# Performance work log

Measured on AMD Instinct MI355X. Metric: run time of the kernel, lower is better.

The kernel has to match this reference:

```python
import jax, jax.numpy as jnp
import numpy as np

N = 10000      # nodes
E = 160000     # edges
D_IN = 512
D_H = 512
P_DROP = 0.2


def _glorot(key, shape):
    lim = float(np.sqrt(6.0 / (shape[0] + shape[1])))
    return jax.random.uniform(key, shape, jnp.float32, -lim, lim)


def setup_inputs() -> dict:
    key = jax.random.key(0)
    ks = jax.random.split(key, 8)
    h = jax.random.normal(ks[0], (N, D_IN), jnp.float32)
    src = jax.random.randint(ks[1], (E,), 0, N)
    dst = jax.random.randint(ks[2], (E,), 0, N)
    edge_weight = jax.random.uniform(ks[3], (E,), jnp.float32)
    W0 = _glorot(ks[4], (D_IN, D_H))
    W1 = _glorot(ks[5], (D_H, D_H))
    W2 = _glorot(ks[6], (D_H, D_H))
    b0 = jnp.zeros((D_H,), jnp.float32)
    b1 = jnp.zeros((D_H,), jnp.float32)
    b2 = jnp.zeros((D_H,), jnp.float32)
    return dict(h=h, src=src, dst=dst, edge_weight=edge_weight,
                W0=W0, b0=b0, W1=W1, b1=b1, W2=W2, b2=b2)


def _dropout(x, key):
    keep = jax.random.bernoulli(key, 1.0 - P_DROP, x.shape)
    return jnp.where(keep, x / (1.0 - P_DROP), 0.0)


def _graph_conv(x, src, dst, ew, W, b, act):
    # DGL GraphConv, norm='both', weight=True, bias=True, with edge_weight.
    ones = jnp.ones((src.shape[0],), x.dtype)
    deg_out = jnp.maximum(jax.ops.segment_sum(ones, src, num_segments=N), 1.0)
    deg_in = jnp.maximum(jax.ops.segment_sum(ones, dst, num_segments=N), 1.0)
    x = x * (deg_out ** -0.5)[:, None]          # src norm
    msg = x[src] * ew[:, None]                  # [E, D] gather + edge weight
    agg = jax.ops.segment_sum(msg, dst, num_segments=N)  # scatter-add
    out = (agg @ W) * (deg_in ** -0.5)[:, None] + b
    return act(out) if act is not None else out


def reference(h, src, dst, edge_weight, W0, b0, W1, b1, W2, b2):
    dk = jax.random.split(jax.random.key(42), 3)
    x = _dropout(h, dk[0])
    x = _graph_conv(x, src, dst, edge_weight, W0, b0, jax.nn.elu)
    x = _dropout(x, dk[1])
    x = _graph_conv(x, src, dst, edge_weight, W1, b1, jax.nn.elu)
    x = _dropout(x, dk[2])
    x = _graph_conv(x, src, dst, edge_weight, W2, b2, None)
    return x
```

## Files before the change

kernel.cpp:

```cpp
#include <hip/hip_runtime.h>
#include <stdint.h>

#define N_NODES 10000
#define N_EDGES 160000
#define D 512
#define TOT (N_NODES * D)
#define M_PAD 10112

typedef _Float16 h8 __attribute__((ext_vector_type(8)));
typedef float f4 __attribute__((ext_vector_type(4)));

__host__ __device__ inline uint32_t rotl32(uint32_t v, int r) {
    return (v << r) | (v >> (32 - r));
}

__host__ __device__ inline void tf2x32(uint32_t k0, uint32_t k1,
                                       uint32_t& x0, uint32_t& x1) {
    uint32_t k2 = k0 ^ k1 ^ 0x1BD11BDAu;
    x0 += k0; x1 += k1;
    x0 += x1; x1 = rotl32(x1, 13); x1 ^= x0;
    x0 += x1; x1 = rotl32(x1, 15); x1 ^= x0;
    x0 += x1; x1 = rotl32(x1, 26); x1 ^= x0;
    x0 += x1; x1 = rotl32(x1,  6); x1 ^= x0;
    x0 += k1; x1 += k2 + 1u;
    x0 += x1; x1 = rotl32(x1, 17); x1 ^= x0;
    x0 += x1; x1 = rotl32(x1, 29); x1 ^= x0;
    x0 += x1; x1 = rotl32(x1, 16); x1 ^= x0;
    x0 += x1; x1 = rotl32(x1, 24); x1 ^= x0;
    x0 += k2; x1 += k0 + 2u;
    x0 += x1; x1 = rotl32(x1, 13); x1 ^= x0;
    x0 += x1; x1 = rotl32(x1, 15); x1 ^= x0;
    x0 += x1; x1 = rotl32(x1, 26); x1 ^= x0;
    x0 += x1; x1 = rotl32(x1,  6); x1 ^= x0;
    x0 += k0; x1 += k1 + 3u;
    x0 += x1; x1 = rotl32(x1, 17); x1 ^= x0;
    x0 += x1; x1 = rotl32(x1, 29); x1 ^= x0;
    x0 += x1; x1 = rotl32(x1, 16); x1 ^= x0;
    x0 += x1; x1 = rotl32(x1, 24); x1 ^= x0;
    x0 += k1; x1 += k2 + 4u;
    x0 += x1; x1 = rotl32(x1, 13); x1 ^= x0;
    x0 += x1; x1 = rotl32(x1, 15); x1 ^= x0;
    x0 += x1; x1 = rotl32(x1, 26); x1 ^= x0;
    x0 += x1; x1 = rotl32(x1,  6); x1 ^= x0;
    x0 += k2; x1 += k0 + 5u;
}

__device__ __forceinline__ float dropout_gate(uint32_t k0, uint32_t k1, uint32_t j) {
    uint32_t c0 = 0u, c1 = j;
    tf2x32(k0, k1, c0, c1);
    uint32_t bits = c0 ^ c1;
    float u = __uint_as_float((bits >> 9) | 0x3f800000u) - 1.0f;
    return (u < 0.8f) ? 1.0f : 0.0f;
}

__device__ __forceinline__ void gl_lds16(const void* g, void* l) {
    __builtin_amdgcn_global_load_lds(
        (const __attribute__((address_space(1))) void*)g,
        (__attribute__((address_space(3))) void*)l, 16, 0, 0);
}

__global__ void hist_kernel(const int* __restrict__ src, const int* __restrict__ dst,
                            int* __restrict__ deg_out, int* __restrict__ deg_in) {
    int e = blockIdx.x * 256 + threadIdx.x;
    if (e >= N_EDGES) return;
    atomicAdd(&deg_out[src[e]], 1);
    atomicAdd(&deg_in[dst[e]], 1);
}

__global__ __launch_bounds__(1024)
void scan_kernel(const int* __restrict__ deg_in, const int* __restrict__ deg_out,
                 int* __restrict__ row_ptr,
                 float* __restrict__ rn_in, float* __restrict__ rn_out) {
    __shared__ int wsum[16];
    __shared__ int base_s;
    int tid = threadIdx.x;
    int lane = tid & 63, wv = tid >> 6;
    if (tid == 0) base_s = 0;
    __syncthreads();
    for (int start = 0; start < N_NODES; start += 1024) {
        int i = start + tid;
        int v = (i < N_NODES) ? deg_in[i] : 0;
        int s = v;
#pragma unroll
        for (int off = 1; off < 64; off <<= 1) {
            int t = __shfl_up(s, off, 64);
            if (lane >= off) s += t;
        }
        if (lane == 63) wsum[wv] = s;
        __syncthreads();
        if (wv == 0 && lane < 16) {
            int ws = wsum[lane];
#pragma unroll
            for (int off = 1; off < 16; off <<= 1) {
                int t = __shfl_up(ws, off, 64);
                if (lane >= off) ws += t;
            }
            wsum[lane] = ws;
        }
        __syncthreads();
        if (i < N_NODES) {
            int prefix = base_s + ((wv > 0) ? wsum[wv - 1] : 0) + (s - v);
            row_ptr[i] = prefix;
            rn_in[i]  = 1.0f / sqrtf(fmaxf((float)v, 1.0f));
            rn_out[i] = 1.0f / sqrtf(fmaxf((float)deg_out[i], 1.0f));
        }
        __syncthreads();
        if (tid == 0) base_s += wsum[15];
        __syncthreads();
    }
    if (tid == 0) row_ptr[N_NODES] = base_s;
}

__global__ void fill_kernel(const int* __restrict__ src, const int* __restrict__ dst,
                            const float* __restrict__ ew, const int* __restrict__ row_ptr,
                            int* __restrict__ cursor,
                            int* __restrict__ csr_src, float* __restrict__ csr_w) {
    int e = blockIdx.x * 256 + threadIdx.x;
    if (e >= N_EDGES) return;
    int v = dst[e];
    int pos = atomicAdd(&cursor[v], 1);
    int idx = row_ptr[v] + pos;
    csr_src[idx] = src[e];
    csr_w[idx] = ew[e];
}

__global__ __launch_bounds__(256)
void wconvert_kernel(const float* __restrict__ W0, const float* __restrict__ W1,
                     const float* __restrict__ W2, _Float16* __restrict__ Wt) {
    __shared__ float tile[64][65];
    const float* W = (blockIdx.z == 0) ? W0 : (blockIdx.z == 1) ? W1 : W2;
    _Float16* T = Wt + (size_t)blockIdx.z * 512 * 512;
    int r0 = blockIdx.y * 64, c0 = blockIdx.x * 64;
    int t = threadIdx.x;
    int c = t & 63, rq = t >> 6;
#pragma unroll
    for (int i = 0; i < 16; ++i) {
        int r = rq + i * 4;
        tile[r][c] = W[(size_t)(r0 + r) * 512 + c0 + c];
    }
    __syncthreads();
    int k = t & 63, nq = t >> 6;
#pragma unroll
    for (int i = 0; i < 16; ++i) {
        int n = nq + i * 4;
        T[(size_t)(c0 + n) * 512 + r0 + k] = (_Float16)tile[k][n];
    }
}

__global__ __launch_bounds__(256)
void dropout_kernel(const float* __restrict__ x, _Float16* __restrict__ y,
                    const float* __restrict__ rn_out, uint32_t k0, uint32_t k1) {
    int t = blockIdx.x * 256 + threadIdx.x;
    int j = t * 4;
    if (j >= TOT) return;
    float4 xv = *(const float4*)&x[j];
    float w = rn_out[j >> 9];
    _Float16 r[4];
    uint32_t jj = (uint32_t)j;
#pragma unroll
    for (int i = 0; i < 4; ++i) {
        float g = dropout_gate(k0, k1, jj + (uint32_t)i);
        float xi = (&xv.x)[i];
        r[i] = (_Float16)(g * (xi / 0.8f) * w);
    }
    *(ushort4*)&y[j] = *(ushort4*)r;
}

__global__ __launch_bounds__(256)
void aggregate_kernel(const _Float16* __restrict__ y, const int* __restrict__ row_ptr,
                      const int* __restrict__ csr_src, const float* __restrict__ csr_w,
                      _Float16* __restrict__ agg) {
    int node = blockIdx.x * 4 + (threadIdx.x >> 6);
    int lane = threadIdx.x & 63;
    if (node >= N_NODES) return;
    int beg = row_ptr[node], end = row_ptr[node + 1];
    float acc[8] = {0, 0, 0, 0, 0, 0, 0, 0};
    int k = beg;
    for (; k + 1 < end; k += 2) {
        int s0 = csr_src[k], s1 = csr_src[k + 1];
        float w0 = csr_w[k], w1 = csr_w[k + 1];
        h8 a = *(const h8*)&y[(size_t)s0 * 512 + lane * 8];
        h8 b = *(const h8*)&y[(size_t)s1 * 512 + lane * 8];
#pragma unroll
        for (int i = 0; i < 8; ++i) acc[i] += w0 * (float)a[i] + w1 * (float)b[i];
    }
    if (k < end) {
        int s0 = csr_src[k];
        float w0 = csr_w[k];
        h8 a = *(const h8*)&y[(size_t)s0 * 512 + lane * 8];
#pragma unroll
        for (int i = 0; i < 8; ++i) acc[i] += w0 * (float)a[i];
    }
    _Float16 r[8];
#pragma unroll
    for (int i = 0; i < 8; ++i) r[i] = (_Float16)acc[i];
    *(h8*)&agg[(size_t)node * 512 + lane * 8] = *(h8*)r;
}

__global__ __launch_bounds__(256)
void gemm_kernel(const _Float16* __restrict__ A, const _Float16* __restrict__ Wt,
                 const float* __restrict__ bias, const float* __restrict__ rn_in,
                 const float* __restrict__ rn_out,
                 _Float16* __restrict__ yout, float* __restrict__ fout,
                 int mode, uint32_t k0, uint32_t k1) {
    __shared__ _Float16 As[128 * 32];
    __shared__ _Float16 Bs[64 * 32];
    int tid = threadIdx.x;
    int wv = tid >> 6, lane = tid & 63;
    int row0 = blockIdx.y * 128, col0 = blockIdx.x * 64;
    int wr = wv >> 1, wc = wv & 1;

    f4 acc[4][2];
#pragma unroll
    for (int i = 0; i < 4; ++i)
#pragma unroll
        for (int j = 0; j < 2; ++j) acc[i][j] = (f4){0.f, 0.f, 0.f, 0.f};

    int kc = (lane & 3) * 8;
    const _Float16* pa0 = A + (size_t)(row0 + 32 * wv + (lane >> 2)) * 512 + kc;
    const _Float16* pa1 = pa0 + 16 * 512;
    const _Float16* pb  = Wt + (size_t)(col0 + 16 * wv + (lane >> 2)) * 512 + kc;
    _Float16* la0 = &As[(32 * wv) * 32];
    _Float16* la1 = &As[(32 * wv + 16) * 32];
    _Float16* lb  = &Bs[(16 * wv) * 32];

    int kf = (lane >> 4) * 8;
    const _Float16* fa = &As[(wr * 64 + (lane & 15)) * 32 + kf];
    const _Float16* fb = &Bs[(wc * 32 + (lane & 15)) * 32 + kf];

    for (int kk = 0; kk < 512; kk += 32) {
        gl_lds16(pa0 + kk, la0);
        gl_lds16(pa1 + kk, la1);
        gl_lds16(pb + kk, lb);
        __syncthreads();
        h8 af[4], bf[2];
#pragma unroll
        for (int mt = 0; mt < 4; ++mt) af[mt] = *(const h8*)(fa + mt * 16 * 32);
#pragma unroll
        for (int nt = 0; nt < 2; ++nt) bf[nt] = *(const h8*)(fb + nt * 16 * 32);
#pragma unroll
        for (int mt = 0; mt < 4; ++mt)
#pragma unroll
            for (int nt = 0; nt < 2; ++nt)
                acc[mt][nt] = __builtin_amdgcn_mfma_f32_16x16x32_f16(
                    af[mt], bf[nt], acc[mt][nt], 0, 0, 0);
        __syncthreads();
    }

    int mbase = row0 + wr * 64;
    int nbase = col0 + wc * 32;
#pragma unroll
    for (int mt = 0; mt < 4; ++mt) {
#pragma unroll
        for (int nt = 0; nt < 2; ++nt) {
            int gr0 = mbase + mt * 16 + (lane >> 4) * 4;
            int gc = nbase + nt * 16 + (lane & 15);
            float bcol = bias[gc];
#pragma unroll
            for (int i = 0; i < 4; ++i) {
                int gr = gr0 + i;
                if (gr >= N_NODES) continue;
                float v = acc[mt][nt][i] * rn_in[gr] + bcol;
                if (mode == 0) {
                    v = (v > 0.f) ? v : expm1f(v);
                    float g = dropout_gate(k0, k1, (uint32_t)(gr * 512 + gc));
                    v = g * (v / 0.8f) * rn_out[gr];
                    yout[(size_t)gr * 512 + gc] = (_Float16)v;
                } else {
                    fout[(size_t)gr * 512 + gc] = v;
                }
            }
        }
    }
}

extern "C" void kernel_launch(void* const* d_in, const int* in_sizes, int n_in,
                              void* d_out, int out_size, void* d_ws, size_t ws_size,
                              hipStream_t stream) {
    const float* h   = (const float*)d_in[0];
    const int*   src = (const int*)d_in[1];
    const int*   dst = (const int*)d_in[2];
    const float* ew  = (const float*)d_in[3];
    const float* W0  = (const float*)d_in[4];
    const float* b0  = (const float*)d_in[5];
    const float* W1  = (const float*)d_in[6];
    const float* b1  = (const float*)d_in[7];
    const float* W2  = (const float*)d_in[8];
    const float* b2  = (const float*)d_in[9];
    const float* bl[3] = {b0, b1, b2};
    float* out = (float*)d_out;

    char* ws = (char*)d_ws;
    _Float16* y16  = (_Float16*)ws; ws += (size_t)TOT * 2;
    _Float16* aggF = (_Float16*)ws; ws += (size_t)M_PAD * 512 * 2;
    _Float16* Wt   = (_Float16*)ws; ws += (size_t)3 * 512 * 512 * 2;
    int* degi_in  = (int*)ws;  ws += N_NODES * 4;
    int* degi_out = (int*)ws;  ws += N_NODES * 4;
    int* row_ptr  = (int*)ws;  ws += (N_NODES + 1) * 4;
    int* cursor   = (int*)ws;  ws += N_NODES * 4;
    int* csr_src  = (int*)ws;  ws += N_EDGES * 4;
    float* csr_w  = (float*)ws; ws += N_EDGES * 4;
    float* rn_in  = (float*)ws; ws += N_NODES * 4;
    float* rn_out = (float*)ws; ws += N_NODES * 4;

    hipMemsetAsync(degi_in, 0, N_NODES * 4, stream);
    hipMemsetAsync(degi_out, 0, N_NODES * 4, stream);
    hipMemsetAsync(cursor, 0, N_NODES * 4, stream);

    hist_kernel<<<(N_EDGES + 255) / 256, 256, 0, stream>>>(src, dst, degi_out, degi_in);
    scan_kernel<<<1, 1024, 0, stream>>>(degi_in, degi_out, row_ptr, rn_in, rn_out);
    fill_kernel<<<(N_EDGES + 255) / 256, 256, 0, stream>>>(src, dst, ew, row_ptr, cursor,
                                                           csr_src, csr_w);
    wconvert_kernel<<<dim3(8, 8, 3), 256, 0, stream>>>(W0, W1, W2, Wt);

    uint32_t dk[3][2];
    for (int i = 0; i < 3; ++i) {
        uint32_t c0 = 0u, c1 = (uint32_t)i;
        tf2x32(0u, 42u, c0, c1);
        dk[i][0] = c0; dk[i][1] = c1;
    }

    dropout_kernel<<<(TOT / 4 + 255) / 256, 256, 0, stream>>>(h, y16, rn_out,
                                                              dk[0][0], dk[0][1]);
    for (int l = 0; l < 3; ++l) {
        aggregate_kernel<<<N_NODES / 4, 256, 0, stream>>>(y16, row_ptr, csr_src,
                                                          csr_w, aggF);
        int mode = (l < 2) ? 0 : 1;
        uint32_t dk0 = (l < 2) ? dk[l + 1][0] : 0u;
        uint32_t dk1 = (l < 2) ? dk[l + 1][1] : 0u;
        gemm_kernel<<<dim3(512 / 64, M_PAD / 128), 256, 0, stream>>>(
            aggF, Wt + (size_t)l * 512 * 512, bl[l], rn_in, rn_out,
            y16, out, mode, dk0, dk1);
    }
}
```

Measured before the change: 327.3 us.

## Pack CSR edges as int2, unroll aggregation by four, widen GEMM K tile

CSR source index and edge weight are interleaved into one int2 array, so the aggregation reads one 8-byte load per edge. The gather loop is unrolled to four edges so more row loads are in flight at once. The GEMM K-tile grows from 32 to 64, halving the number of barrier-separated iterations at the cost of more LDS. The three memsets are merged into one by placing the counters next to each other.

```diff
diff --git a/kernel.cpp b/kernel.cpp
--- a/kernel.cpp
+++ b/kernel.cpp
@@ -113,15 +113,13 @@
 
 __global__ void fill_kernel(const int* __restrict__ src, const int* __restrict__ dst,
                             const float* __restrict__ ew, const int* __restrict__ row_ptr,
-                            int* __restrict__ cursor,
-                            int* __restrict__ csr_src, float* __restrict__ csr_w) {
+                            int* __restrict__ cursor, int2* __restrict__ csr) {
     int e = blockIdx.x * 256 + threadIdx.x;
     if (e >= N_EDGES) return;
     int v = dst[e];
     int pos = atomicAdd(&cursor[v], 1);
     int idx = row_ptr[v] + pos;
-    csr_src[idx] = src[e];
-    csr_w[idx] = ew[e];
+    csr[idx] = make_int2(src[e], __float_as_int(ew[e]));
 }
 
 __global__ __launch_bounds__(256)
@@ -168,26 +166,30 @@
 
 __global__ __launch_bounds__(256)
 void aggregate_kernel(const _Float16* __restrict__ y, const int* __restrict__ row_ptr,
-                      const int* __restrict__ csr_src, const float* __restrict__ csr_w,
-                      _Float16* __restrict__ agg) {
+                      const int2* __restrict__ csr, _Float16* __restrict__ agg) {
     int node = blockIdx.x * 4 + (threadIdx.x >> 6);
     int lane = threadIdx.x & 63;
     if (node >= N_NODES) return;
     int beg = row_ptr[node], end = row_ptr[node + 1];
     float acc[8] = {0, 0, 0, 0, 0, 0, 0, 0};
     int k = beg;
-    for (; k + 1 < end; k += 2) {
-        int s0 = csr_src[k], s1 = csr_src[k + 1];
-        float w0 = csr_w[k], w1 = csr_w[k + 1];
-        h8 a = *(const h8*)&y[(size_t)s0 * 512 + lane * 8];
-        h8 b = *(const h8*)&y[(size_t)s1 * 512 + lane * 8];
-#pragma unroll
-        for (int i = 0; i < 8; ++i) acc[i] += w0 * (float)a[i] + w1 * (float)b[i];
-    }
-    if (k < end) {
-        int s0 = csr_src[k];
-        float w0 = csr_w[k];
-        h8 a = *(const h8*)&y[(size_t)s0 * 512 + lane * 8];
+    for (; k + 3 < end; k += 4) {
+        int2 e0 = csr[k], e1 = csr[k + 1], e2 = csr[k + 2], e3 = csr[k + 3];
+        h8 a0 = *(const h8*)&y[(size_t)e0.x * 512 + lane * 8];
+        h8 a1 = *(const h8*)&y[(size_t)e1.x * 512 + lane * 8];
+        h8 a2 = *(const h8*)&y[(size_t)e2.x * 512 + lane * 8];
+        h8 a3 = *(const h8*)&y[(size_t)e3.x * 512 + lane * 8];
+        float w0 = __int_as_float(e0.y), w1 = __int_as_float(e1.y);
+        float w2 = __int_as_float(e2.y), w3 = __int_as_float(e3.y);
+#pragma unroll
+        for (int i = 0; i < 8; ++i)
+            acc[i] += w0 * (float)a0[i] + w1 * (float)a1[i]
+                    + w2 * (float)a2[i] + w3 * (float)a3[i];
+    }
+    for (; k < end; ++k) {
+        int2 e0 = csr[k];
+        float w0 = __int_as_float(e0.y);
+        h8 a = *(const h8*)&y[(size_t)e0.x * 512 + lane * 8];
 #pragma unroll
         for (int i = 0; i < 8; ++i) acc[i] += w0 * (float)a[i];
     }
@@ -197,14 +199,15 @@
     *(h8*)&agg[(size_t)node * 512 + lane * 8] = *(h8*)r;
 }
 
+#define GBK 64
 __global__ __launch_bounds__(256)
 void gemm_kernel(const _Float16* __restrict__ A, const _Float16* __restrict__ Wt,
                  const float* __restrict__ bias, const float* __restrict__ rn_in,
                  const float* __restrict__ rn_out,
                  _Float16* __restrict__ yout, float* __restrict__ fout,
                  int mode, uint32_t k0, uint32_t k1) {
-    __shared__ _Float16 As[128 * 32];
-    __shared__ _Float16 Bs[64 * 32];
+    __shared__ _Float16 As[128 * GBK];
+    __shared__ _Float16 Bs[64 * GBK];
     int tid = threadIdx.x;
     int wv = tid >> 6, lane = tid & 63;
     int row0 = blockIdx.y * 128, col0 = blockIdx.x * 64;
@@ -216,34 +219,41 @@
 #pragma unroll
         for (int j = 0; j < 2; ++j) acc[i][j] = (f4){0.f, 0.f, 0.f, 0.f};
 
-    int kc = (lane & 3) * 8;
-    const _Float16* pa0 = A + (size_t)(row0 + 32 * wv + (lane >> 2)) * 512 + kc;
-    const _Float16* pa1 = pa0 + 16 * 512;
-    const _Float16* pb  = Wt + (size_t)(col0 + 16 * wv + (lane >> 2)) * 512 + kc;
-    _Float16* la0 = &As[(32 * wv) * 32];
-    _Float16* la1 = &As[(32 * wv + 16) * 32];
-    _Float16* lb  = &Bs[(16 * wv) * 32];
+    int srow = lane >> 3;
+    int skc = (lane & 7) * 8;
+    const _Float16* pa = A + (size_t)(row0 + 32 * wv + srow) * 512 + skc;
+    const _Float16* pb = Wt + (size_t)(col0 + 16 * wv + srow) * 512 + skc;
+    _Float16* la = &As[(32 * wv) * GBK];
+    _Float16* lb = &Bs[(16 * wv) * GBK];
 
     int kf = (lane >> 4) * 8;
-    const _Float16* fa = &As[(wr * 64 + (lane & 15)) * 32 + kf];
-    const _Float16* fb = &Bs[(wc * 32 + (lane & 15)) * 32 + kf];
-
-    for (int kk = 0; kk < 512; kk += 32) {
-        gl_lds16(pa0 + kk, la0);
-        gl_lds16(pa1 + kk, la1);
-        gl_lds16(pb + kk, lb);
-        __syncthreads();
-        h8 af[4], bf[2];
-#pragma unroll
-        for (int mt = 0; mt < 4; ++mt) af[mt] = *(const h8*)(fa + mt * 16 * 32);
-#pragma unroll
-        for (int nt = 0; nt < 2; ++nt) bf[nt] = *(const h8*)(fb + nt * 16 * 32);
-#pragma unroll
-        for (int mt = 0; mt < 4; ++mt)
+    const _Float16* fa = &As[(wr * 64 + (lane & 15)) * GBK + kf];
+    const _Float16* fb = &Bs[(wc * 32 + (lane & 15)) * GBK + kf];
+
+    for (int kk = 0; kk < 512; kk += GBK) {
+#pragma unroll
+        for (int r = 0; r < 4; ++r)
+            gl_lds16(pa + (size_t)r * 8 * 512 + kk, la + (8 * r) * GBK);
+#pragma unroll
+        for (int r = 0; r < 2; ++r)
+            gl_lds16(pb + (size_t)r * 8 * 512 + kk, lb + (8 * r) * GBK);
+        __syncthreads();
+#pragma unroll
+        for (int ks = 0; ks < 2; ++ks) {
+            h8 af[4], bf[2];
+#pragma unroll
+            for (int mt = 0; mt < 4; ++mt)
+                af[mt] = *(const h8*)(fa + mt * 16 * GBK + ks * 32);
 #pragma unroll
             for (int nt = 0; nt < 2; ++nt)
-                acc[mt][nt] = __builtin_amdgcn_mfma_f32_16x16x32_f16(
-                    af[mt], bf[nt], acc[mt][nt], 0, 0, 0);
+                bf[nt] = *(const h8*)(fb + nt * 16 * GBK + ks * 32);
+#pragma unroll
+            for (int mt = 0; mt < 4; ++mt)
+#pragma unroll
+                for (int nt = 0; nt < 2; ++nt)
+                    acc[mt][nt] = __builtin_amdgcn_mfma_f32_16x16x32_f16(
+                        af[mt], bf[nt], acc[mt][nt], 0, 0, 0);
+        }
         __syncthreads();
     }
 
@@ -296,21 +306,19 @@
     _Float16* Wt   = (_Float16*)ws; ws += (size_t)3 * 512 * 512 * 2;
     int* degi_in  = (int*)ws;  ws += N_NODES * 4;
     int* degi_out = (int*)ws;  ws += N_NODES * 4;
+    int* cursor   = (int*)ws;  ws += N_NODES * 4;
     int* row_ptr  = (int*)ws;  ws += (N_NODES + 1) * 4;
-    int* cursor   = (int*)ws;  ws += N_NODES * 4;
-    int* csr_src  = (int*)ws;  ws += N_EDGES * 4;
-    float* csr_w  = (float*)ws; ws += N_EDGES * 4;
+    ws = (char*)(((uintptr_t)ws + 15) & ~(uintptr_t)15);
+    int2* csr     = (int2*)ws; ws += (size_t)N_EDGES * 8;
     float* rn_in  = (float*)ws; ws += N_NODES * 4;
     float* rn_out = (float*)ws; ws += N_NODES * 4;
 
-    hipMemsetAsync(degi_in, 0, N_NODES * 4, stream);
-    hipMemsetAsync(degi_out, 0, N_NODES * 4, stream);
-    hipMemsetAsync(cursor, 0, N_NODES * 4, stream);
+    hipMemsetAsync(degi_in, 0, 3 * N_NODES * 4, stream);
 
     hist_kernel<<<(N_EDGES + 255) / 256, 256, 0, stream>>>(src, dst, degi_out, degi_in);
     scan_kernel<<<1, 1024, 0, stream>>>(degi_in, degi_out, row_ptr, rn_in, rn_out);
-    fill_kernel<<<(N_EDGES + 255) / 256, 256, 0, stream>>>(src, dst, ew, row_ptr, cursor,
-                                                           csr_src, csr_w);
+    fill_kernel<<<(N_EDGES + 255) / 256, 256, 0, stream>>>(src, dst, ew, row_ptr,
+                                                           cursor, csr);
     wconvert_kernel<<<dim3(8, 8, 3), 256, 0, stream>>>(W0, W1, W2, Wt);
 
     uint32_t dk[3][2];
@@ -323,8 +331,7 @@
     dropout_kernel<<<(TOT / 4 + 255) / 256, 256, 0, stream>>>(h, y16, rn_out,
                                                               dk[0][0], dk[0][1]);
     for (int l = 0; l < 3; ++l) {
-        aggregate_kernel<<<N_NODES / 4, 256, 0, stream>>>(y16, row_ptr, csr_src,
-                                                          csr_w, aggF);
+        aggregate_kernel<<<N_NODES / 4, 256, 0, stream>>>(y16, row_ptr, csr, aggF);
         int mode = (l < 2) ? 0 : 1;
         uint32_t dk0 = (l < 2) ? dk[l + 1][0] : 0u;
         uint32_t dk1 = (l < 2) ? dk[l + 1][1] : 0u;
```

New measurement: 310.5 us. -5.2%, faster.
